# Optimization experiments

Hardware: AMD Instinct MI355X
Metric: run time of the kernel (lower is better)

Reference implementation:

```python
import jax, jax.numpy as jnp
import numpy as np

C, G, K, PAD = 64, 8, 9, 1  # channels, deformable groups, 3x3 taps, padding


def conv2d(x, w, b):
    y = jax.lax.conv_general_dilated(x, w, (1, 1), [(PAD, PAD), (PAD, PAD)],
                                     dimension_numbers=('NCHW', 'OIHW', 'NCHW'))
    return y + b[None, :, None, None]


def deform_conv(x, offset, w, b, groups):
    # x: [B,Cin,H,W]; offset: [B, 2*groups*K, H, W] laid out as (g, k, (dy,dx))
    B, Cin, H, W = x.shape
    Cg = Cin // groups
    dt = x.dtype
    off = offset.reshape(B, groups, K, 2, H, W)
    dy, dx = off[:, :, :, 0], off[:, :, :, 1]                  # [B,G,K,H,W]
    ky, kx = jnp.meshgrid(jnp.arange(3, dtype=dt), jnp.arange(3, dtype=dt), indexing='ij')
    ky, kx = ky.reshape(K), kx.reshape(K)
    grid_y = jnp.arange(H, dtype=dt)[None, None, None, :, None]
    grid_x = jnp.arange(W, dtype=dt)[None, None, None, None, :]
    py = grid_y - PAD + ky[None, None, :, None, None] + dy      # sample rows
    px = grid_x - PAD + kx[None, None, :, None, None] + dx      # sample cols

    y0 = jnp.floor(py)
    x0 = jnp.floor(px)
    xf = x.reshape(B, groups, Cg, H * W)

    def corner(yi, xi):
        valid = ((yi >= 0) & (yi <= H - 1) & (xi >= 0) & (xi <= W - 1)).astype(dt)
        idx = (jnp.clip(yi, 0, H - 1).astype(jnp.int32) * W
               + jnp.clip(xi, 0, W - 1).astype(jnp.int32)).reshape(B, groups, K * H * W)
        g = jax.vmap(jax.vmap(lambda f, i: f[:, i]))(xf, idx)   # [B,G,Cg,K*H*W]
        return g, valid.reshape(B, groups, 1, K * H * W)

    wy1 = (py - y0).reshape(B, groups, 1, -1)
    wx1 = (px - x0).reshape(B, groups, 1, -1)
    wy0, wx0 = 1.0 - wy1, 1.0 - wx1

    g00, v00 = corner(y0, x0)
    acc = g00 * (v00 * wy0 * wx0)
    g01, v01 = corner(y0, x0 + 1)
    acc = acc + g01 * (v01 * wy0 * wx1)
    g10, v10 = corner(y0 + 1, x0)
    acc = acc + g10 * (v10 * wy1 * wx0)
    g11, v11 = corner(y0 + 1, x0 + 1)
    acc = acc + g11 * (v11 * wy1 * wx1)

    sampled = acc.reshape(B, Cin, K, H, W)                      # G*Cg == Cin
    out = jnp.einsum('bckhw,ock->bohw', sampled, w.reshape(w.shape[0], Cin, K))
    return out + b[None, :, None, None]


def setup_inputs() -> dict:
    key = jax.random.key(0)
    ks = jax.random.split(key, 9)
    B, H, W = 2, 192, 192
    f = lambda k, s, sc=0.05: jax.random.normal(k, s, dtype=jnp.float32) * sc
    return dict(
        previous_features=jax.random.normal(ks[0], (B, C, H, W), dtype=jnp.float32),
        offsets=jax.random.normal(ks[1], (B, C, H, W), dtype=jnp.float32),
        w_off=f(ks[2], (2 * G * K, C, 3, 3), 0.01),
        b_off=jnp.zeros((2 * G * K,), jnp.float32),
        w_dcn=f(ks[3], (C, C, 3, 3)),
        b_dcn=f(ks[4], (C,)),
        w_r1=f(ks[5], (C, 2 * C, 3, 3)),
        b_r1=f(ks[6], (C,)),
        w_r2=f(ks[7], (C, C, 3, 3)),
        b_r2=f(ks[8], (C,)),
    )


def reference(previous_features, offsets, w_off, b_off, w_dcn, b_dcn, w_r1, b_r1, w_r2, b_r2):
    off = conv2d(offsets, w_off, b_off)                         # extra_offset_mask path
    aligned = deform_conv(previous_features, off, w_dcn, b_dcn, G)
    r = jnp.concatenate([aligned, previous_features], axis=1)
    r = jax.nn.leaky_relu(conv2d(r, w_r1, b_r1), 0.1)
    r = jax.nn.leaky_relu(conv2d(r, w_r2, b_r2), 0.1)
    return aligned + r
```

## Files before the change

kernel.cpp:

```cpp
#include <hip/hip_runtime.h>
#include <hip/hip_bf16.h>
#include <cstdint>
#include <cstddef>

constexpr int B_ = 2;
constexpr int HH = 192, WW = 192, HW_ = HH * WW;
constexpr int HP = 194, WPAD = 200;

typedef short bf16x8 __attribute__((ext_vector_type(8)));
typedef short s16x4  __attribute__((ext_vector_type(4)));
typedef float f32x4  __attribute__((ext_vector_type(4)));
typedef unsigned int u32x4 __attribute__((ext_vector_type(4)));

typedef __attribute__((address_space(1))) const void GLB;
typedef __attribute__((address_space(3))) void LDS;

__device__ __forceinline__ float bf2f(unsigned short h) {
  union { unsigned u; float f; } v; v.u = (unsigned)h << 16; return v.f;
}
__device__ __forceinline__ unsigned short f2bf(float f) {
  union { float f; unsigned u; } v; v.f = f;
  unsigned u = v.u;
  u += 0x7fffu + ((u >> 16) & 1u);
  return (unsigned short)(u >> 16);
}
__device__ __forceinline__ float leaky(float v) { return fmaxf(v, 0.1f * v); }

__global__ __launch_bounds__(256) void borderzero(unsigned short* __restrict__ offs_t,
                                                  unsigned short* __restrict__ concat_t,
                                                  unsigned short* __restrict__ r1_t)
{
  int tid = blockIdx.x * 256 + threadIdx.x;
  if (tid >= B_ * HP * WPAD) return;
  int x = tid % WPAD, y = (tid / WPAD) % HP, b = tid / (HP * WPAD);
  bool border = (y == 0) || (y >= 193) || (x == 0) || (x >= 193);
  if (!border) return;
  size_t px = (size_t)(b * HP + y) * WPAD + x;
  u32x4 z4 = {0u, 0u, 0u, 0u};
  u32x4* p0 = (u32x4*)(offs_t   + px * 64);
  u32x4* p1 = (u32x4*)(concat_t + px * 128);
  u32x4* p2 = (u32x4*)(r1_t     + px * 64);
  #pragma unroll
  for (int i = 0; i < 8; ++i)  p0[i] = z4;
  #pragma unroll
  for (int i = 0; i < 16; ++i) p1[i] = z4;
  #pragma unroll
  for (int i = 0; i < 8; ++i)  p2[i] = z4;
}

template<int DSTC>
__global__ __launch_bounds__(256) void to_nhwc(const float* __restrict__ src,
                                               unsigned short* __restrict__ dst,
                                               int coff)
{
  __shared__ float tile[16][65];
  int t = threadIdx.x;
  int xc = blockIdx.x * 16;
  int y = blockIdx.y % HH, b = blockIdx.y / HH;
  #pragma unroll
  for (int cp = 0; cp < 4; ++cp) {
    int c = cp * 16 + (t >> 4);
    tile[t & 15][c] = src[((size_t)(b * 64 + c) * HH + y) * WW + xc + (t & 15)];
  }
  __syncthreads();
  int x = t >> 4, c4 = (t & 15) * 4;
  s16x4 s;
  #pragma unroll
  for (int j = 0; j < 4; ++j) s[j] = (short)f2bf(tile[x][c4 + j]);
  *(s16x4*)&dst[((size_t)(b * HP + y + 1) * WPAD + xc + x + 1) * DSTC + coff + c4] = s;
}

__global__ __launch_bounds__(256) void prep_prev(const float* __restrict__ src,
                                                 unsigned short* __restrict__ concatT,
                                                 unsigned short* __restrict__ gp)
{
  __shared__ float tile[16][65];
  int t = threadIdx.x;
  int xc = blockIdx.x * 16;
  int y = blockIdx.y % HH, b = blockIdx.y / HH;
  #pragma unroll
  for (int cp = 0; cp < 4; ++cp) {
    int c = cp * 16 + (t >> 4);
    tile[t & 15][c] = src[((size_t)(b * 64 + c) * HH + y) * WW + xc + (t & 15)];
  }
  __syncthreads();
  int x = t >> 4, c4 = (t & 15) * 4;
  s16x4 s;
  #pragma unroll
  for (int j = 0; j < 4; ++j) s[j] = (short)f2bf(tile[x][c4 + j]);
  *(s16x4*)&concatT[((size_t)(b * HP + y + 1) * WPAD + xc + x + 1) * 128 + 64 + c4] = s;
  int g = c4 >> 3, co = c4 & 7;
  *(s16x4*)&gp[((size_t)(b * 8 + g) * HW_ + (size_t)y * WW + xc + x) * 8 + co] = s;
}

__global__ __launch_bounds__(256) void wxform(
    const float* __restrict__ w_off, const float* __restrict__ w_dcn,
    const float* __restrict__ w_r1,  const float* __restrict__ w_r2,
    unsigned short* __restrict__ wOffB, unsigned short* __restrict__ wDcnB,
    unsigned short* __restrict__ wR1B,  unsigned short* __restrict__ wR2B)
{
  int tid = blockIdx.x * 256 + threadIdx.x;
  const float* src; unsigned short* dst; int CI, CO, idx; bool dosw = true;
  if (tid < 82944)            { src = w_off; dst = wOffB; CI = 64;  CO = 144; idx = tid; }
  else if (tid < 119808)      { src = w_dcn; dst = wDcnB; CI = 64;  CO = 64;  idx = tid - 82944; dosw = false; }
  else if (tid < 193536)      { src = w_r1;  dst = wR1B;  CI = 128; CO = 64;  idx = tid - 119808; }
  else                        { src = w_r2;  dst = wR2B;  CI = 64;  CO = 64;  idx = tid - 193536; }
  int ci = idx % CI;
  int k  = (idx / CI) % 9;
  int o  = idx / (CI * 9);
  int pci = dosw ? (((((ci >> 3) ^ (o & 7))) << 3) | (ci & 7)) : ci;
  dst[((size_t)k * CO + o) * CI + pci] = f2bf(src[((size_t)o * CI + ci) * 9 + k]);
}

template<int CIN, int COUT, int NF, bool LEAKY_, int OUTMODE, bool DBUF>
__global__ __launch_bounds__(256, 4) void conv_mfma(
    const unsigned short* __restrict__ inT,
    const unsigned short* __restrict__ wS,
    const float* __restrict__ bias,
    const unsigned short* __restrict__ resid,
    void* __restrict__ outp)
{
  constexpr int CPP  = CIN / 8;
  constexpr int TPX  = 72;
  constexpr int NCH  = TPX * CPP;
  constexpr int RPR  = NCH / 64;
  constexpr int NREG = 3 * RPR;
  constexpr int WSZ  = NF * 16 * CIN;
  constexpr int WCH  = WSZ / 8;
  static_assert(WCH % 128 == 0, "staging must use full waves");
  __shared__ __align__(16) unsigned short tile[3 * TPX * CIN];
  __shared__ __align__(16) unsigned short wlds[(DBUF ? 2 : 1) * WSZ];

  const int t = threadIdx.x;
  const int l = t & 63, wv = t >> 6;
  const int lr = l & 15, lq = l >> 4, lk = lq * 8;

  constexpr int NWG = 3 * 384;
  int lin = blockIdx.x + 3 * blockIdx.y;
  int swz = (lin & 7) * (NWG / 8) + (lin >> 3);
  int xq = swz % 3, yy = swz / 3;
  int y = yy % HH, b = yy / HH;
  int x0 = xq * 64;
  const int co0 = blockIdx.z * (NF * 16);

  {
    const unsigned short* base = inT + ((size_t)(b * HP + y) * WPAD + x0) * CIN;
    for (int r = wv; r < NREG; r += 4) {
      int row = r / RPR;
      int rr  = r % RPR;
      int d   = rr * 64 + l;
      int p   = d / CPP;
      int cj  = d % CPP;
      int sc  = p * CPP + (cj ^ (p & (CPP - 1)));
      const unsigned short* src = base + (size_t)row * WPAD * CIN + (size_t)sc * 8;
      unsigned short* dst = &tile[(size_t)(row * NCH + rr * 64) * 8];
      __builtin_amdgcn_global_load_lds((GLB*)src, (LDS*)dst, 16, 0, 0);
    }
  }
  {
    const unsigned short* srcb = wS + (size_t)co0 * CIN;
    for (int r = t; r < WCH; r += 256)
      __builtin_amdgcn_global_load_lds((GLB*)(srcb + (size_t)r * 8),
                                       (LDS*)(&wlds[(size_t)r * 8]), 16, 0, 0);
  }
  __syncthreads();

  f32x4 acc[NF];
  #pragma unroll
  for (int f = 0; f < NF; ++f) acc[f] = f32x4{0.f, 0.f, 0.f, 0.f};

  #pragma unroll
  for (int k = 0; k < 9; ++k) {
    const int ky = k / 3, kx = k % 3;
    if (DBUF && k < 8) {
      const unsigned short* srcb = wS + (size_t)(k + 1) * COUT * CIN + (size_t)co0 * CIN;
      unsigned short* db = &wlds[(size_t)((k + 1) & 1) * WSZ];
      for (int r = t; r < WCH; r += 256)
        __builtin_amdgcn_global_load_lds((GLB*)(srcb + (size_t)r * 8),
                                         (LDS*)(db + (size_t)r * 8), 16, 0, 0);
    }
    {
      const unsigned short* wb = &wlds[DBUF ? (size_t)(k & 1) * WSZ : 0];
      const int px = wv * 16 + lr + kx;
      #pragma unroll
      for (int c = 0; c < CIN; c += 32) {
        int cj = (c + lk) >> 3;
        bf16x8 pf = *(const bf16x8*)
            &tile[(size_t)(ky * NCH + px * CPP + (cj ^ (px & (CPP - 1)))) * 8];
        #pragma unroll
        for (int f = 0; f < NF; ++f) {
          int co = f * 16 + lr;
          bf16x8 wf = *(const bf16x8*)&wb[(size_t)co * CIN + ((cj ^ (co & 7)) << 3)];
          if (OUTMODE == 0)
            acc[f] = __builtin_amdgcn_mfma_f32_16x16x32_bf16(pf, wf, acc[f], 0, 0, 0);
          else
            acc[f] = __builtin_amdgcn_mfma_f32_16x16x32_bf16(wf, pf, acc[f], 0, 0, 0);
        }
      }
    }
    if (DBUF) {
      __syncthreads();
    } else if (k < 8) {
      __syncthreads();
      const unsigned short* srcb = wS + (size_t)(k + 1) * COUT * CIN + (size_t)co0 * CIN;
      for (int r = t; r < WCH; r += 256)
        __builtin_amdgcn_global_load_lds((GLB*)(srcb + (size_t)r * 8),
                                         (LDS*)(&wlds[(size_t)r * 8]), 16, 0, 0);
      __syncthreads();
    }
  }

  if (OUTMODE == 0) {
    int xs = x0 + wv * 16 + lq * 4;
    #pragma unroll
    for (int f = 0; f < NF; ++f) {
      int coG = co0 + f * 16 + lr;
      float bv = bias[coG];
      s16x4 s;
      #pragma unroll
      for (int j = 0; j < 4; ++j) {
        float v = acc[f][j] + bv;
        if (LEAKY_) v = leaky(v);
        s[j] = (short)f2bf(v);
      }
      *(s16x4*)((unsigned short*)outp + ((size_t)(b * COUT + coG) * HH + y) * WW + xs) = s;
    }
  } else if (OUTMODE == 1) {
    int x = x0 + wv * 16 + lr;
    #pragma unroll
    for (int f = 0; f < NF; ++f) {
      int co = f * 16 + lq * 4;
      f32x4 bv = *(const f32x4*)&bias[co];
      s16x4 s;
      #pragma unroll
      for (int j = 0; j < 4; ++j) {
        float v = acc[f][j] + bv[j];
        if (LEAKY_) v = leaky(v);
        s[j] = (short)f2bf(v);
      }
      *(s16x4*)((unsigned short*)outp + ((size_t)(b * HP + y + 1) * WPAD + x + 1) * 64 + co) = s;
    }
  } else {
    int x = x0 + wv * 16 + lr;
    const unsigned short* rbase = resid + ((size_t)(b * HP + y + 1) * WPAD + x + 1) * 128;
    float* ob = (float*)outp + (size_t)b * 64 * HW_ + (size_t)y * WW + x;
    #pragma unroll
    for (int f = 0; f < NF; ++f) {
      int cob = f * 16 + lq * 4;
      f32x4 bv = *(const f32x4*)&bias[cob];
      s16x4 rv = *(const s16x4*)&rbase[cob];
      #pragma unroll
      for (int j = 0; j < 4; ++j) {
        float v = acc[f][j] + bv[j];
        if (LEAKY_) v = leaky(v);
        v += bf2f((unsigned short)rv[j]);
        ob[(size_t)(cob + j) * HW_] = v;
      }
    }
  }
}

__global__ __launch_bounds__(256, 4) void deform_mfma(
    const unsigned short* __restrict__ gp,
    const unsigned short* __restrict__ off,
    const unsigned short* __restrict__ wD,
    const float* __restrict__ bias,
    unsigned short* __restrict__ concatT)
{
  __shared__ __align__(16) unsigned short win[2048 * 8];
  const int t = threadIdx.x;
  const int l = t & 63, wv = t >> 6;
  const int lr = l & 15, lq = l >> 4;

  int lin = blockIdx.x;
  int swz = (lin & 7) * 144 + (lin >> 3);
  int xt = swz % 6;
  int rest = swz / 6;
  int yp = rest % 96, b = rest / 96;
  int Y = yp * 2, x0 = xt * 32;
  int yrow = Y + (wv >> 1);
  int xpix = x0 + (wv & 1) * 16 + lr;

  const int wy = Y - 2, wx = x0 - 3;
  const unsigned short* gpb = gp + (size_t)b * 8 * HW_ * 8;

  #pragma unroll
  for (int i = 0; i < 8; ++i) {
    int p  = t + i * 256;
    int g  = min(p / 241, 7);
    int rc = p - g * 241;
    int rcc = min(rc, 239);
    int r  = rcc / 40;
    int c  = rcc - r * 40;
    int yr = min(max(wy + r, 0), HH - 1);
    int xc = min(max(wx + c, 0), WW - 1);
    const unsigned short* src = gpb + ((size_t)g * HW_ + (size_t)yr * WW + xc) * 8;
    __builtin_amdgcn_global_load_lds((GLB*)src,
                                     (LDS*)(win + (size_t)p * 8), 16, 0, 0);
  }

  unsigned dd[2][9];
  #pragma unroll
  for (int gi = 0; gi < 2; ++gi) {
    int g = lq + gi * 4;
    const unsigned short* op = off + ((size_t)(b * 144 + g * 18) * HH + yrow) * WW + xpix;
    #pragma unroll
    for (int k = 0; k < 9; ++k) {
      unsigned dyv = op[(size_t)(2 * k) * HW_];
      unsigned dxv = op[(size_t)(2 * k + 1) * HW_];
      dd[gi][k] = dyv | (dxv << 16);
    }
  }

  __syncthreads();

  f32x4 acc[4];
  #pragma unroll
  for (int f = 0; f < 4; ++f) acc[f] = f32x4{0.f, 0.f, 0.f, 0.f};

  #pragma unroll
  for (int k = 0; k < 9; ++k) {
    const int ky = k / 3, kx = k % 3;
    bf16x8 pf0, pf1;
    #pragma unroll
    for (int gi = 0; gi < 2; ++gi) {
      int g = lq + gi * 4;
      float dyv = bf2f((unsigned short)(dd[gi][k] & 0xffffu));
      float dxv = bf2f((unsigned short)(dd[gi][k] >> 16));
      float py = (float)(yrow - 1 + ky) + dyv;
      float px = (float)(xpix - 1 + kx) + dxv;
      float fy0 = floorf(py), fx0 = floorf(px);
      float wy1 = py - fy0, wx1 = px - fx0;
      float wy0 = 1.f - wy1, wx0 = 1.f - wx1;
      bool vy0 = (fy0 >= 0.f)  && (fy0 <= 191.f);
      bool vy1 = (fy0 >= -1.f) && (fy0 <= 190.f);
      bool vx0 = (fx0 >= 0.f)  && (fx0 <= 191.f);
      bool vx1 = (fx0 >= -1.f) && (fx0 <= 190.f);
      float c00 = (vy0 && vx0) ? wy0 * wx0 : 0.f;
      float c01 = (vy0 && vx1) ? wy0 * wx1 : 0.f;
      float c10 = (vy1 && vx0) ? wy1 * wx0 : 0.f;
      float c11 = (vy1 && vx1) ? wy1 * wx1 : 0.f;
      int iy0 = (int)fminf(fmaxf(fy0, 0.f), 191.f);
      int iy1 = (int)fminf(fmaxf(fy0 + 1.f, 0.f), 191.f);
      int ix0 = (int)fminf(fmaxf(fx0, 0.f), 191.f);
      int ix1 = (int)fminf(fmaxf(fx0 + 1.f, 0.f), 191.f);
      bool inw = (iy0 >= wy) && (iy1 <= wy + 5) && (ix0 >= wx) && (ix1 <= wx + 39);
      int ry0 = min(max(iy0 - wy, 0), 5), ry1 = min(max(iy1 - wy, 0), 5);
      int rx0 = min(max(ix0 - wx, 0), 39), rx1 = min(max(ix1 - wx, 0), 39);
      const unsigned short* wg = win + (size_t)g * (241 * 8);
      bf16x8 v00 = *(const bf16x8*)(wg + ((size_t)ry0 * 40 + rx0) * 8);
      bf16x8 v01 = *(const bf16x8*)(wg + ((size_t)ry0 * 40 + rx1) * 8);
      bf16x8 v10 = *(const bf16x8*)(wg + ((size_t)ry1 * 40 + rx0) * 8);
      bf16x8 v11 = *(const bf16x8*)(wg + ((size_t)ry1 * 40 + rx1) * 8);
      if (!__all((int)inw)) {
        if (!inw) {
          const unsigned short* bb = gpb + (size_t)g * HW_ * 8;
          v00 = *(const bf16x8*)(bb + ((size_t)iy0 * WW + ix0) * 8);
          v01 = *(const bf16x8*)(bb + ((size_t)iy0 * WW + ix1) * 8);
          v10 = *(const bf16x8*)(bb + ((size_t)iy1 * WW + ix0) * 8);
          v11 = *(const bf16x8*)(bb + ((size_t)iy1 * WW + ix1) * 8);
        }
      }
      bf16x8 sv;
      #pragma unroll
      for (int j = 0; j < 8; ++j) {
        float s = bf2f((unsigned short)v00[j]) * c00
                + bf2f((unsigned short)v01[j]) * c01
                + bf2f((unsigned short)v10[j]) * c10
                + bf2f((unsigned short)v11[j]) * c11;
        sv[j] = (short)f2bf(s);
      }
      if (gi == 0) pf0 = sv; else pf1 = sv;
    }
    #pragma unroll
    for (int f = 0; f < 4; ++f) {
      bf16x8 wf = *(const bf16x8*)&wD[((size_t)k * 64 + f * 16 + lr) * 64 + lq * 8];
      acc[f] = __builtin_amdgcn_mfma_f32_16x16x32_bf16(wf, pf0, acc[f], 0, 0, 0);
    }
    #pragma unroll
    for (int f = 0; f < 4; ++f) {
      bf16x8 wf = *(const bf16x8*)&wD[((size_t)k * 64 + f * 16 + lr) * 64 + 32 + lq * 8];
      acc[f] = __builtin_amdgcn_mfma_f32_16x16x32_bf16(wf, pf1, acc[f], 0, 0, 0);
    }
  }

  unsigned short* outc = concatT + (size_t)b * HP * WPAD * 128;
  #pragma unroll
  for (int f = 0; f < 4; ++f) {
    int co = f * 16 + lq * 4;
    f32x4 bv = *(const f32x4*)&bias[co];
    s16x4 s;
    #pragma unroll
    for (int j = 0; j < 4; ++j) s[j] = (short)f2bf(acc[f][j] + bv[j]);
    *(s16x4*)&outc[((size_t)(yrow + 1) * WPAD + xpix + 1) * 128 + co] = s;
  }
}

extern "C" void kernel_launch(void* const* d_in, const int* in_sizes, int n_in,
                              void* d_out, int out_size, void* d_ws, size_t ws_size,
                              hipStream_t stream)
{
  const float* prev  = (const float*)d_in[0];
  const float* offin = (const float*)d_in[1];
  const float* w_off = (const float*)d_in[2];
  const float* b_off = (const float*)d_in[3];
  const float* w_dcn = (const float*)d_in[4];
  const float* b_dcn = (const float*)d_in[5];
  const float* w_r1  = (const float*)d_in[6];
  const float* b_r1  = (const float*)d_in[7];
  const float* w_r2  = (const float*)d_in[8];
  const float* b_r2  = (const float*)d_in[9];
  float* out = (float*)d_out;

  char* p = (char*)d_ws;
  unsigned short* offs_t   = (unsigned short*)p; p += (size_t)B_ * HP * WPAD * 64 * 2;
  unsigned short* concat_t = (unsigned short*)p; p += (size_t)B_ * HP * WPAD * 128 * 2;
  unsigned short* r1_t     = (unsigned short*)p; p += (size_t)B_ * HP * WPAD * 64 * 2;
  unsigned short* offf     = (unsigned short*)p; p += (size_t)B_ * 144 * HW_ * 2;
  unsigned short* wOffB    = (unsigned short*)p; p += 144 * 576 * 2;
  unsigned short* wDcnB    = (unsigned short*)p; p += 64 * 576 * 2;
  unsigned short* wR1B     = (unsigned short*)p; p += 64 * 1152 * 2;
  unsigned short* wR2B     = (unsigned short*)p; p += 64 * 576 * 2;
  unsigned short* gp = offs_t;

  borderzero<<<(B_ * HP * WPAD + 255) / 256, 256, 0, stream>>>(offs_t, concat_t, r1_t);

  wxform<<<900, 256, 0, stream>>>(w_off, w_dcn, w_r1, w_r2, wOffB, wDcnB, wR1B, wR2B);
  to_nhwc<64><<<dim3(12, 384), 256, 0, stream>>>(offin, offs_t, 0);

  conv_mfma<64, 144, 3, false, 0, true><<<dim3(3, 384, 3), 256, 0, stream>>>(
      offs_t, wOffB, b_off, nullptr, offf);

  prep_prev<<<dim3(12, 384), 256, 0, stream>>>(prev, concat_t, gp);

  deform_mfma<<<1152, 256, 0, stream>>>(gp, offf, wDcnB, b_dcn, concat_t);

  conv_mfma<128, 64, 4, true, 1, false><<<dim3(3, 384, 1), 256, 0, stream>>>(
      concat_t, wR1B, b_r1, nullptr, r1_t);

  conv_mfma<64, 64, 4, true, 2, true><<<dim3(3, 384, 1), 256, 0, stream>>>(
      r1_t, wR2B, b_r2, concat_t, out);
}
```

Before: 152.7 us.

## Fuse prep kernels into one launch and split refine convs over output channels

Merges the border-zero, weight-transform and offset NHWC transpose kernels into a single launch dispatched by block index, which saves launch overhead. The two refinement convolutions now split the 64 output channels across two grid z-slices (NF 2 instead of 4). This doubles the block count and enables double buffering for the first refine conv. The output epilogues add the co0 channel base to support the split, at the cost of loading the input tile redundantly once per channel half.

```diff
diff --git a/kernel.cpp b/kernel.cpp
--- a/kernel.cpp
+++ b/kernel.cpp
@@ -26,48 +26,64 @@
 }
 __device__ __forceinline__ float leaky(float v) { return fmaxf(v, 0.1f * v); }
 
-__global__ __launch_bounds__(256) void borderzero(unsigned short* __restrict__ offs_t,
-                                                  unsigned short* __restrict__ concat_t,
-                                                  unsigned short* __restrict__ r1_t)
-{
-  int tid = blockIdx.x * 256 + threadIdx.x;
-  if (tid >= B_ * HP * WPAD) return;
-  int x = tid % WPAD, y = (tid / WPAD) % HP, b = tid / (HP * WPAD);
-  bool border = (y == 0) || (y >= 193) || (x == 0) || (x >= 193);
-  if (!border) return;
-  size_t px = (size_t)(b * HP + y) * WPAD + x;
-  u32x4 z4 = {0u, 0u, 0u, 0u};
-  u32x4* p0 = (u32x4*)(offs_t   + px * 64);
-  u32x4* p1 = (u32x4*)(concat_t + px * 128);
-  u32x4* p2 = (u32x4*)(r1_t     + px * 64);
-  #pragma unroll
-  for (int i = 0; i < 8; ++i)  p0[i] = z4;
-  #pragma unroll
-  for (int i = 0; i < 16; ++i) p1[i] = z4;
-  #pragma unroll
-  for (int i = 0; i < 8; ++i)  p2[i] = z4;
-}
-
-template<int DSTC>
-__global__ __launch_bounds__(256) void to_nhwc(const float* __restrict__ src,
-                                               unsigned short* __restrict__ dst,
-                                               int coff)
+__global__ __launch_bounds__(256) void prep0(
+    const float* __restrict__ offin,
+    const float* __restrict__ w_off, const float* __restrict__ w_dcn,
+    const float* __restrict__ w_r1,  const float* __restrict__ w_r2,
+    unsigned short* __restrict__ offs_t, unsigned short* __restrict__ concat_t,
+    unsigned short* __restrict__ r1_t,
+    unsigned short* __restrict__ wOffB, unsigned short* __restrict__ wDcnB,
+    unsigned short* __restrict__ wR1B,  unsigned short* __restrict__ wR2B)
 {
   __shared__ float tile[16][65];
+  int bid = blockIdx.x;
   int t = threadIdx.x;
-  int xc = blockIdx.x * 16;
-  int y = blockIdx.y % HH, b = blockIdx.y / HH;
-  #pragma unroll
-  for (int cp = 0; cp < 4; ++cp) {
-    int c = cp * 16 + (t >> 4);
-    tile[t & 15][c] = src[((size_t)(b * 64 + c) * HH + y) * WW + xc + (t & 15)];
-  }
-  __syncthreads();
-  int x = t >> 4, c4 = (t & 15) * 4;
-  s16x4 s;
-  #pragma unroll
-  for (int j = 0; j < 4; ++j) s[j] = (short)f2bf(tile[x][c4 + j]);
-  *(s16x4*)&dst[((size_t)(b * HP + y + 1) * WPAD + xc + x + 1) * DSTC + coff + c4] = s;
+
+  if (bid < 4608) {
+    int bx = bid % 12, by = bid / 12;
+    int xc = bx * 16;
+    int y = by % HH, b = by / HH;
+    #pragma unroll
+    for (int cp = 0; cp < 4; ++cp) {
+      int c = cp * 16 + (t >> 4);
+      tile[t & 15][c] = offin[((size_t)(b * 64 + c) * HH + y) * WW + xc + (t & 15)];
+    }
+    __syncthreads();
+    int x = t >> 4, c4 = (t & 15) * 4;
+    s16x4 s;
+    #pragma unroll
+    for (int j = 0; j < 4; ++j) s[j] = (short)f2bf(tile[x][c4 + j]);
+    *(s16x4*)&offs_t[((size_t)(b * HP + y + 1) * WPAD + xc + x + 1) * 64 + c4] = s;
+  } else if (bid < 5508) {
+    int tid = (bid - 4608) * 256 + t;
+    const float* src; unsigned short* dst; int CI, CO, idx; bool dosw = true;
+    if (tid < 82944)       { src = w_off; dst = wOffB; CI = 64;  CO = 144; idx = tid; }
+    else if (tid < 119808) { src = w_dcn; dst = wDcnB; CI = 64;  CO = 64;  idx = tid - 82944; dosw = false; }
+    else if (tid < 193536) { src = w_r1;  dst = wR1B;  CI = 128; CO = 64;  idx = tid - 119808; }
+    else                   { src = w_r2;  dst = wR2B;  CI = 64;  CO = 64;  idx = tid - 193536; }
+    int ci = idx % CI;
+    int k  = (idx / CI) % 9;
+    int o  = idx / (CI * 9);
+    int pci = dosw ? (((((ci >> 3) ^ (o & 7))) << 3) | (ci & 7)) : ci;
+    dst[((size_t)k * CO + o) * CI + pci] = f2bf(src[((size_t)o * CI + ci) * 9 + k]);
+  } else {
+    int tid = (bid - 5508) * 256 + t;
+    if (tid >= B_ * HP * WPAD) return;
+    int x = tid % WPAD, y = (tid / WPAD) % HP, b = tid / (HP * WPAD);
+    bool border = (y == 0) || (y >= 193) || (x == 0) || (x >= 193);
+    if (!border) return;
+    size_t px = (size_t)(b * HP + y) * WPAD + x;
+    u32x4 z4 = {0u, 0u, 0u, 0u};
+    u32x4* p0 = (u32x4*)(offs_t   + px * 64);
+    u32x4* p1 = (u32x4*)(concat_t + px * 128);
+    u32x4* p2 = (u32x4*)(r1_t     + px * 64);
+    #pragma unroll
+    for (int i = 0; i < 8; ++i)  p0[i] = z4;
+    #pragma unroll
+    for (int i = 0; i < 16; ++i) p1[i] = z4;
+    #pragma unroll
+    for (int i = 0; i < 8; ++i)  p2[i] = z4;
+  }
 }
 
 __global__ __launch_bounds__(256) void prep_prev(const float* __restrict__ src,
@@ -91,25 +107,6 @@
   *(s16x4*)&concatT[((size_t)(b * HP + y + 1) * WPAD + xc + x + 1) * 128 + 64 + c4] = s;
   int g = c4 >> 3, co = c4 & 7;
   *(s16x4*)&gp[((size_t)(b * 8 + g) * HW_ + (size_t)y * WW + xc + x) * 8 + co] = s;
-}
-
-__global__ __launch_bounds__(256) void wxform(
-    const float* __restrict__ w_off, const float* __restrict__ w_dcn,
-    const float* __restrict__ w_r1,  const float* __restrict__ w_r2,
-    unsigned short* __restrict__ wOffB, unsigned short* __restrict__ wDcnB,
-    unsigned short* __restrict__ wR1B,  unsigned short* __restrict__ wR2B)
-{
-  int tid = blockIdx.x * 256 + threadIdx.x;
-  const float* src; unsigned short* dst; int CI, CO, idx; bool dosw = true;
-  if (tid < 82944)            { src = w_off; dst = wOffB; CI = 64;  CO = 144; idx = tid; }
-  else if (tid < 119808)      { src = w_dcn; dst = wDcnB; CI = 64;  CO = 64;  idx = tid - 82944; dosw = false; }
-  else if (tid < 193536)      { src = w_r1;  dst = wR1B;  CI = 128; CO = 64;  idx = tid - 119808; }
-  else                        { src = w_r2;  dst = wR2B;  CI = 64;  CO = 64;  idx = tid - 193536; }
-  int ci = idx % CI;
-  int k  = (idx / CI) % 9;
-  int o  = idx / (CI * 9);
-  int pci = dosw ? (((((ci >> 3) ^ (o & 7))) << 3) | (ci & 7)) : ci;
-  dst[((size_t)k * CO + o) * CI + pci] = f2bf(src[((size_t)o * CI + ci) * 9 + k]);
 }
 
 template<int CIN, int COUT, int NF, bool LEAKY_, int OUTMODE, bool DBUF>
@@ -229,8 +226,8 @@
     int x = x0 + wv * 16 + lr;
     #pragma unroll
     for (int f = 0; f < NF; ++f) {
-      int co = f * 16 + lq * 4;
-      f32x4 bv = *(const f32x4*)&bias[co];
+      int coG = co0 + f * 16 + lq * 4;
+      f32x4 bv = *(const f32x4*)&bias[coG];
       s16x4 s;
       #pragma unroll
       for (int j = 0; j < 4; ++j) {
@@ -238,7 +235,7 @@
         if (LEAKY_) v = leaky(v);
         s[j] = (short)f2bf(v);
       }
-      *(s16x4*)((unsigned short*)outp + ((size_t)(b * HP + y + 1) * WPAD + x + 1) * 64 + co) = s;
+      *(s16x4*)((unsigned short*)outp + ((size_t)(b * HP + y + 1) * WPAD + x + 1) * 64 + coG) = s;
     }
   } else {
     int x = x0 + wv * 16 + lr;
@@ -246,15 +243,15 @@
     float* ob = (float*)outp + (size_t)b * 64 * HW_ + (size_t)y * WW + x;
     #pragma unroll
     for (int f = 0; f < NF; ++f) {
-      int cob = f * 16 + lq * 4;
-      f32x4 bv = *(const f32x4*)&bias[cob];
-      s16x4 rv = *(const s16x4*)&rbase[cob];
+      int cobG = co0 + f * 16 + lq * 4;
+      f32x4 bv = *(const f32x4*)&bias[cobG];
+      s16x4 rv = *(const s16x4*)&rbase[cobG];
       #pragma unroll
       for (int j = 0; j < 4; ++j) {
         float v = acc[f][j] + bv[j];
         if (LEAKY_) v = leaky(v);
         v += bf2f((unsigned short)rv[j]);
-        ob[(size_t)(cob + j) * HW_] = v;
+        ob[(size_t)(cobG + j) * HW_] = v;
       }
     }
   }
@@ -423,10 +420,9 @@
   unsigned short* wR2B     = (unsigned short*)p; p += 64 * 576 * 2;
   unsigned short* gp = offs_t;
 
-  borderzero<<<(B_ * HP * WPAD + 255) / 256, 256, 0, stream>>>(offs_t, concat_t, r1_t);
-
-  wxform<<<900, 256, 0, stream>>>(w_off, w_dcn, w_r1, w_r2, wOffB, wDcnB, wR1B, wR2B);
-  to_nhwc<64><<<dim3(12, 384), 256, 0, stream>>>(offin, offs_t, 0);
+  prep0<<<5812, 256, 0, stream>>>(offin, w_off, w_dcn, w_r1, w_r2,
+                                  offs_t, concat_t, r1_t,
+                                  wOffB, wDcnB, wR1B, wR2B);
 
   conv_mfma<64, 144, 3, false, 0, true><<<dim3(3, 384, 3), 256, 0, stream>>>(
       offs_t, wOffB, b_off, nullptr, offf);
@@ -435,9 +431,9 @@
 
   deform_mfma<<<1152, 256, 0, stream>>>(gp, offf, wDcnB, b_dcn, concat_t);
 
-  conv_mfma<128, 64, 4, true, 1, false><<<dim3(3, 384, 1), 256, 0, stream>>>(
+  conv_mfma<128, 64, 2, true, 1, true><<<dim3(3, 384, 2), 256, 0, stream>>>(
       concat_t, wR1B, b_r1, nullptr, r1_t);
 
-  conv_mfma<64, 64, 4, true, 2, true><<<dim3(3, 384, 1), 256, 0, stream>>>(
+  conv_mfma<64, 64, 2, true, 2, true><<<dim3(3, 384, 2), 256, 0, stream>>>(
       r1_t, wR2B, b_r2, concat_t, out);
 }
```

After: 156.7 us. +2.6%, slower.
